# Kernel optimization log

Hardware: AMD Instinct MI355X
Metric: run time of the kernel (lower is better)

## Reference

```python
import jax, jax.numpy as jnp
import numpy as np

B, WS, DIM, HEADS, AGENT, PS = 128, 14, 256, 8, 49, 7
N = WS * WS


def conv(x, w, b, pad, groups=1):
    y = jax.lax.conv_general_dilated(x, w, (1, 1), [(pad, pad), (pad, pad)],
                                     dimension_numbers=('NCHW', 'OIHW', 'NCHW'),
                                     feature_group_count=groups)
    return y + b[None, :, None, None]


def bilinear_resize(x, oh, ow):
    # F.interpolate(mode='bilinear', align_corners=False) on last two dims
    ih, iw = x.shape[-2], x.shape[-1]
    def grid(ni, no):
        pos = np.maximum((np.arange(no) + 0.5) * (ni / no) - 0.5, 0.0)
        i0 = np.minimum(np.floor(pos).astype(np.int32), ni - 1)
        i1 = np.minimum(i0 + 1, ni - 1)
        return i0, i1, (pos - i0).astype(np.float32)
    i0h, i1h, lh = grid(ih, oh)
    i0w, i1w, lw = grid(iw, ow)
    xh = x[..., i0h, :] * (1.0 - lh)[:, None] + x[..., i1h, :] * lh[:, None]
    return xh[..., i0w] * (1.0 - lw) + xh[..., i1w] * lw


def rel_pos_index(h, w):
    coords = np.stack(np.meshgrid(np.arange(h), np.arange(w), indexing='ij')).reshape(2, -1)
    rel = (coords[:, :, None] - coords[:, None, :]).transpose(1, 2, 0).copy()
    rel[..., 0] += h - 1
    rel[..., 1] += w - 1
    rel[..., 0] *= 2 * w - 1
    return rel.sum(-1)  # (h*w, h*w)


def cbam(x, caa1_w, caa1_b, caa2_w, caa2_b, cam1_w, cam1_b, cam2_w, cam2_b, sa_w, sa_b):
    # ChannelAttention: both conv stacks act on 1x1 pooled maps -> only kernel centers matter
    avgp = x.mean((2, 3))
    t1 = jax.nn.relu(jnp.einsum('oi,bi->bo', caa1_w[:, :, 1, 1], avgp) + caa1_b)
    y1 = jax.nn.sigmoid(jnp.einsum('oi,bi->bo', caa2_w[:, :, 1, 1], t1) + caa2_b)
    mxp = x.max((2, 3))
    t2 = jax.nn.relu(jnp.einsum('oi,bi->bo', cam1_w[:, :, 0, 0], mxp) + cam1_b)
    y2 = jax.nn.sigmoid(jnp.einsum('oi,bi->bo', cam2_w[:, :, 0, 0], t2) + cam2_b)
    x = jax.nn.sigmoid(y1 + y2)[:, :, None, None] * x
    # Spatial attention
    mask = jnp.concatenate([x.mean(1, keepdims=True), x.max(1, keepdims=True)], axis=1)
    mask = jax.nn.sigmoid(conv(mask, sa_w, sa_b, 4))
    return x * mask


def chan_inter(x, ci1_w, ci1_b, bn_g, bn_b, ci2_w, ci2_b):
    # AdaptiveAvgPool2d(1) then 5x5 convs on 1x1 maps -> kernel-center matmuls; BN in eval mode
    p = x.mean((2, 3))
    t = jnp.einsum('oi,bi->bo', ci1_w[:, :, 2, 2], p) + ci1_b
    t = jax.nn.relu(bn_g * t * (1.0 / np.sqrt(1.0 + 1e-5)) + bn_b)
    return jnp.einsum('oi,bi->bo', ci2_w[:, :, 2, 2], t) + ci2_b


def setup_inputs() -> dict:
    key = jax.random.key(0)
    ks = jax.random.split(key, 40)
    d, r = DIM, DIM // 16
    p = lambda i, shape, s=0.02: jax.random.normal(ks[i], shape, jnp.float32) * s
    return {
        'x': jax.random.normal(ks[0], (B, N, d), jnp.float32),
        'h': WS,
        'w': WS,
        'lka_w': p(1, (3 * d, 1, 5, 5)), 'lka_b': p(2, (3 * d,)),
        'conv5_w': p(3, (d, d, 5, 5)), 'conv5_b': p(4, (d,)),
        'caa1_w': p(5, (r, d, 3, 3)), 'caa1_b': p(6, (r,)),
        'caa2_w': p(7, (d, r, 3, 3)), 'caa2_b': p(8, (d,)),
        'cam1_w': p(9, (r, d, 1, 1)), 'cam1_b': p(10, (r,)),
        'cam2_w': p(11, (d, r, 1, 1)), 'cam2_b': p(12, (d,)),
        'sa_w': p(13, (1, 2, 9, 9)), 'sa_b': p(14, (1,)),
        'ci1_w': p(15, (r, d, 5, 5)), 'ci1_b': p(16, (r,)),
        'bn_g': jnp.ones((r,), jnp.float32), 'bn_b': jnp.zeros((r,), jnp.float32),
        'ci2_w': p(17, (d, r, 5, 5)), 'ci2_b': p(18, (d,)),
        'rpb_table': p(19, ((2 * WS - 1) * (2 * WS - 1), HEADS)),
        'an_bias': p(20, (HEADS, AGENT, 7, 7)), 'na_bias': p(21, (HEADS, AGENT, 7, 7)),
        'ah_bias': p(22, (1, HEADS, AGENT, WS, 1)), 'aw_bias': p(23, (1, HEADS, AGENT, 1, WS)),
        'ha_bias': p(24, (1, HEADS, WS, 1, AGENT)), 'wa_bias': p(25, (1, HEADS, 1, WS, AGENT)),
        'dwc_w': p(26, (d, 1, 5, 5)), 'dwc_b': p(27, (d,)),
        'proj_w': p(28, (d, d)), 'proj_b': p(29, (d,)),
    }


def reference(x, h, w, lka_w, lka_b, conv5_w, conv5_b, caa1_w, caa1_b, caa2_w, caa2_b,
              cam1_w, cam1_b, cam2_w, cam2_b, sa_w, sa_b, ci1_w, ci1_b, bn_g, bn_b,
              ci2_w, ci2_b, rpb_table, an_bias, na_bias, ah_bias, aw_bias, ha_bias,
              wa_bias, dwc_w, dwc_b, proj_w, proj_b):
    b, n, c = x.shape
    heads, agent, ps = HEADS, AGENT, PS
    hd = c // heads
    scale = hd ** (-0.5)

    xc = jnp.transpose(x.reshape(b, h, w, c), (0, 3, 1, 2))  # (b,c,h,w)
    y = conv(xc, lka_w, lka_b, 2, groups=c)                   # depthwise, 3 outputs/group
    k_raw, v_raw, q_raw = y[:, :c], y[:, c:2 * c], y[:, 2 * c:]

    # v branch: conv5 then raw reshape-scramble (faithful to torch .reshape of NCHW), then CBAM
    v5 = jnp.transpose(conv(v_raw, conv5_w, conv5_b, 2).reshape(b, h, w, c), (0, 3, 1, 2))
    vc = cbam(v5, caa1_w, caa1_b, caa2_w, caa2_b, cam1_w, cam1_b, cam2_w, cam2_b, sa_w, sa_b)
    v_feat = jnp.transpose(vc.reshape(b, c, n), (0, 2, 1))    # (b,n,c)

    # adaptive avg/max pool 14->7 == exact 2x2 pooling
    at = q_raw.reshape(b, c, ps, h // ps, ps, w // ps).mean((3, 5)).reshape(b, c, agent).transpose(0, 2, 1)
    atk = k_raw.reshape(b, c, ps, h // ps, ps, w // ps).max((3, 5)).reshape(b, c, agent).transpose(0, 2, 1)

    # raw row-major reshapes of (b,c,h,w) into (b,n,heads,hd): faithful to torch
    q = q_raw.reshape(b, n, heads, hd).transpose(0, 2, 1, 3) * scale
    k = k_raw.reshape(b, n, heads, hd).transpose(0, 2, 1, 3)
    v = v_raw.reshape(b, n, heads, hd).transpose(0, 2, 1, 3)
    v1 = v_feat.reshape(b, n, heads, hd).transpose(0, 2, 1, 3)

    # full window attention with relative position bias
    idx = rel_pos_index(h, w)
    rpb = rpb_table[idx.reshape(-1)].reshape(n, n, heads).transpose(2, 0, 1)
    attn = jax.nn.softmax(jnp.einsum('bhid,bhjd->bhij', q, k) + rpb[None])
    x1 = jnp.einsum('bhij,bhjd->bhid', attn, v).transpose(0, 2, 1, 3).reshape(b, n, c)

    ar = x1.transpose(0, 2, 1).reshape(b, c, h, w)
    cmap = chan_inter(ar, ci1_w, ci1_b, bn_g, bn_b, ci2_w, ci2_b)  # (b,c)
    conv_x2 = jax.nn.sigmoid(cmap)[:, :, None, None] * jnp.transpose(q.reshape(b, h, w, c), (0, 3, 1, 2))

    # agent attention
    at_h = at.reshape(b, agent, heads, hd).transpose(0, 2, 1, 3)
    atk_h = atk.reshape(b, agent, heads, hd).transpose(0, 2, 1, 3)
    pb = bilinear_resize(an_bias, h, w).reshape(1, heads, agent, n) \
         + (ah_bias + aw_bias).reshape(1, heads, agent, n)
    agent_attn = jax.nn.softmax(jnp.einsum('bhad,bhnd->bhan', at_h * scale, k) + pb)
    agent_attn1 = jax.nn.softmax(jnp.einsum('bhad,bhnd->bhan', atk_h * scale, q) + pb)
    agent_v = jnp.einsum('bhan,bhnd->bhad', agent_attn, v1) + jnp.einsum('bhan,bhnd->bhad', agent_attn1, v)

    ab = bilinear_resize(na_bias, h, w).reshape(1, heads, agent, n).transpose(0, 1, 3, 2) \
         + (ha_bias + wa_bias).reshape(1, heads, n, agent)
    q_attn = jax.nn.softmax(jnp.einsum('bhnd,bhad->bhna', q * scale, at_h) + ab)
    k_attn = jax.nn.softmax(jnp.einsum('bhnd,bhad->bhna', k * scale, atk_h) + ab)
    xo = jnp.einsum('bhna,bhad->bhnd', q_attn + k_attn, agent_v).transpose(0, 2, 1, 3).reshape(b, n, c)

    xo = xo + jnp.transpose(conv(conv_x2, dwc_w, dwc_b, 2, groups=c), (0, 2, 3, 1)).reshape(b, n, c)
    qc = jnp.transpose(q.transpose(0, 2, 1, 3).reshape(b, h, w, c), (0, 3, 1, 2))
    xo = xo + jnp.transpose(conv(qc, dwc_w, dwc_b, 2, groups=c), (0, 2, 3, 1)).reshape(b, n, c)

    return xo @ proj_w.T + proj_b
```

## Files before the change

### kernel.cpp

```cpp
#include <hip/hip_runtime.h>

#define NB    128
#define NC    256
#define NPOS  196
#define NHEAD 8
#define NAG   49
#define YSTR  150528
#define VOFF  50176
#define QOFF  100352
#define SCL   0.17677669529663687f

#define WS_Y    0u
#define WS_V5   19267584u
#define WS_AT   25690112u
#define WS_ATK  27295744u
#define WS_CHG  28901376u
#define WS_CMAP 28934144u
#define WS_PBT  28966912u
#define WS_AB   29043744u
#define WS_X1S  29120576u
#define WS_AGV  29153344u
#define WS_XO   30758976u
#define WS_WT   37181504u
#define WS_CWT  37247040u

typedef __attribute__((ext_vector_type(8))) _Float16 half8;
typedef __attribute__((ext_vector_type(8))) short short8;
typedef __attribute__((ext_vector_type(4))) short short4v;
typedef __attribute__((ext_vector_type(4))) float f32x4;
typedef unsigned short ushort_t;
typedef unsigned int uint_t;

__device__ __forceinline__ float sigmoidf_(float x){ return 1.0f/(1.0f+__expf(-x)); }

__device__ __forceinline__ ushort_t f2h(float x){
  _Float16 h = (_Float16)x; return __builtin_bit_cast(ushort_t, h);
}
__device__ __forceinline__ float h2f(ushort_t u){
  return (float)__builtin_bit_cast(_Float16, u);
}

__device__ __forceinline__ float bilin7(const float* __restrict__ src, int i, int j){
  float pi = fmaxf(0.5f*(float)i - 0.25f, 0.f);
  int i0 = (int)pi; if (i0 > 6) i0 = 6;
  int i1 = i0 + 1;  if (i1 > 6) i1 = 6;
  float li = pi - (float)i0;
  float pj = fmaxf(0.5f*(float)j - 0.25f, 0.f);
  int j0 = (int)pj; if (j0 > 6) j0 = 6;
  int j1 = j0 + 1;  if (j1 > 6) j1 = 6;
  float lj = pj - (float)j0;
  float v00 = src[i0*7+j0], v01 = src[i0*7+j1];
  float v10 = src[i1*7+j0], v11 = src[i1*7+j1];
  float t0 = v00*(1.f-lj) + v01*lj;
  float t1 = v10*(1.f-lj) + v11*lj;
  return t0*(1.f-li) + t1*li;
}

__device__ __forceinline__ void conv5x5_row(const float* __restrict__ plane, int r,
                                            const float* __restrict__ w25, float* acc14){
  #pragma unroll
  for (int di = 0; di < 5; ++di){
    const float4* pr = (const float4*)(plane + (r+di)*20);
    float4 p0 = pr[0], p1 = pr[1], p2 = pr[2], p3 = pr[3], p4 = pr[4];
    float row[20] = {p0.x,p0.y,p0.z,p0.w, p1.x,p1.y,p1.z,p1.w, p2.x,p2.y,p2.z,p2.w,
                     p3.x,p3.y,p3.z,p3.w, p4.x,p4.y,p4.z,p4.w};
    #pragma unroll
    for (int dj = 0; dj < 5; ++dj){
      float w = w25[di*5+dj];
      #pragma unroll
      for (int j = 0; j < 14; ++j) acc14[j] = fmaf(row[j+dj], w, acc14[j]);
    }
  }
}

__global__ void k_pbab(const float* __restrict__ an, const float* __restrict__ ah,
                       const float* __restrict__ aw, const float* __restrict__ na,
                       const float* __restrict__ ha, const float* __restrict__ wa,
                       float* __restrict__ PBT, float* __restrict__ AB){
  int bid = blockIdx.x;
  int which = (bid >= 301);
  int t = (which ? bid - 301 : bid)*256 + threadIdx.x;
  if (t >= NHEAD*NPOS*NAG) return;
  int a = t % NAG;
  int r = t / NAG;
  int n = r % NPOS;
  int h = r / NPOS;
  int i = n/14, j = n - (n/14)*14;
  if (!which){
    float v = bilin7(an + ((size_t)h*NAG + a)*49, i, j);
    v += ah[((size_t)h*NAG + a)*14 + i] + aw[((size_t)h*NAG + a)*14 + j];
    PBT[t] = v;
  } else {
    float v = bilin7(na + ((size_t)h*NAG + a)*49, i, j);
    v += ha[((size_t)h*14 + i)*NAG + a] + wa[((size_t)h*14 + j)*NAG + a];
    AB[t] = v;
  }
}

__global__ void k_wt(const float* __restrict__ pw, float* __restrict__ WT){
  int t = blockIdx.x*256 + threadIdx.x;
  if (t >= 65536) return;
  int k = t >> 8, c = t & 255;
  WT[t] = pw[c*256 + k];
}

__global__ void k_cw2(const float* __restrict__ cw, ushort_t* __restrict__ Wh){
  int t = blockIdx.x*256 + threadIdx.x;
  if (t >= 1638400) return;
  int ci = t & 255;
  int r  = t >> 8;
  int co = r & 255;
  int tap = r >> 8;
  Wh[t] = f2h(cw[((size_t)co*256 + ci)*25 + tap]);
}

__global__ __launch_bounds__(256) void k_lka(const float* __restrict__ x, const float* __restrict__ lw,
                                             const float* __restrict__ lb, float* __restrict__ Y){
  int b = blockIdx.x >> 3, gb = blockIdx.x & 7;
  int g0 = gb*32;
  __shared__ __align__(16) float pl[32*360];
  int tid = threadIdx.x;
  for (int t = tid; t < 32*360; t += 256) pl[t] = 0.f;
  __syncthreads();
  for (int t = tid; t < 32*196; t += 256){
    int gl = t & 31, s = t >> 5;
    int i = s/14, j = s - i*14;
    pl[gl*360 + (i+2)*20 + j + 2] = x[((size_t)b*196 + s)*256 + g0 + gl];
  }
  __syncthreads();
  for (int t = tid; t < 96*14; t += 256){
    int ocl = t/14, r = t - ocl*14;
    int o  = g0*3 + ocl;
    int gl = ocl/3;
    float w25[25];
    #pragma unroll
    for (int u = 0; u < 25; ++u) w25[u] = lw[o*25 + u];
    float acc[14];
    float bv = lb[o];
    #pragma unroll
    for (int j = 0; j < 14; ++j) acc[j] = bv;
    conv5x5_row(&pl[gl*360], r, w25, acc);
    float* dst = Y + ((size_t)b*768 + o)*196 + r*14;
    #pragma unroll
    for (int j = 0; j < 14; ++j) dst[j] = acc[j];
  }
}

__global__ __launch_bounds__(256, 2) void k_conv5(const float* __restrict__ Y,
    const ushort_t* __restrict__ Wh, const float* __restrict__ cb, float* __restrict__ V5){
  int b = blockIdx.x >> 2, cog = blockIdx.x & 3;
  int co0 = cog*64;
  __shared__ __align__(16) ushort_t Pt[360*40];
  __shared__ __align__(16) ushort_t Wsm[2*5*64*40];
  float* T = (float*)Wsm;
  int tid  = threadIdx.x;
  int lane = tid & 63, wv = tid >> 6;
  int mrow = lane & 15, quad = lane >> 4;

  for (int t = tid; t < 7200; t += 256) ((uint_t*)Pt)[t] = 0;

  int prow[4];
  #pragma unroll
  for (int mt = 0; mt < 4; ++mt){
    int s = wv*64 + mt*16 + mrow;
    int p0 = 0;
    if (s < 196){ int i = s/14, j = s - i*14; p0 = i*20 + j; }
    prow[mt] = p0;
  }

  f32x4 acc[4][4];
  #pragma unroll
  for (int mt = 0; mt < 4; ++mt)
    #pragma unroll
    for (int nt = 0; nt < 4; ++nt) acc[mt][nt] = (f32x4){0.f,0.f,0.f,0.f};

  const float* src = Y + (size_t)b*YSTR + VOFF;
  int wco = tid >> 2, wpart = tid & 3;
  const ushort_t* wbase = Wh + ((size_t)(co0 + wco))*256 + wpart*8;

  short8 wreg[5];
  #pragma unroll
  for (int tp = 0; tp < 5; ++tp)
    wreg[tp] = *(const short8*)(wbase + (size_t)tp*65536);

  #pragma unroll 1
  for (int cc = 0; cc < 8; ++cc){
    __syncthreads();
    for (int t = tid; t < 784; t += 256){
      int pos = t >> 2, ch = t & 3;
      int i = pos/14, j = pos - i*14;
      int p = (i+2)*20 + j + 2;
      const float* s0 = src + (size_t)(cc*32 + ch*8)*196 + pos;
      short8 pk;
      #pragma unroll
      for (int e = 0; e < 4; ++e){
        float v0 = s0[(2*e)*196];
        float v1 = s0[(2*e+1)*196];
        pk[2*e]   = (short)f2h(v0);
        pk[2*e+1] = (short)f2h(v1);
      }
      *(short8*)&Pt[p*40 + ch*8] = pk;
    }
    #pragma unroll 1
    for (int di = 0; di < 5; ++di){
      int u = cc*5 + di;
      ushort_t* wbuf = Wsm + (u & 1)*12800;
      #pragma unroll
      for (int tp = 0; tp < 5; ++tp)
        *(short8*)&wbuf[(tp*64 + wco)*40 + wpart*8] = wreg[tp];
      if (u < 39){
        int di1 = di + 1, cc1 = cc;
        if (di1 == 5){ di1 = 0; ++cc1; }
        #pragma unroll
        for (int tp = 0; tp < 5; ++tp)
          wreg[tp] = *(const short8*)(wbase + (size_t)(di1*5 + tp)*65536 + cc1*32);
      }
      __syncthreads();
      #pragma unroll
      for (int dj = 0; dj < 5; ++dj){
        half8 a[4], bb[4];
        #pragma unroll
        for (int nt = 0; nt < 4; ++nt){
          int co = nt*16 + mrow;
          bb[nt] = *(const half8*)&wbuf[(dj*64 + co)*40 + quad*8];
        }
        #pragma unroll
        for (int mt = 0; mt < 4; ++mt){
          int p = prow[mt] + di*20 + dj;
          a[mt] = *(const half8*)&Pt[p*40 + quad*8];
        }
        #pragma unroll
        for (int mt = 0; mt < 4; ++mt)
          #pragma unroll
          for (int nt = 0; nt < 4; ++nt)
            acc[mt][nt] = __builtin_amdgcn_mfma_f32_16x16x32_f16(a[mt], bb[nt], acc[mt][nt], 0, 0, 0);
      }
    }
  }

  #pragma unroll
  for (int hf = 0; hf < 2; ++hf){
    __syncthreads();
    #pragma unroll
    for (int ntl = 0; ntl < 2; ++ntl){
      int nt = hf*2 + ntl;
      int col = ntl*16 + mrow;
      #pragma unroll
      for (int mt = 0; mt < 4; ++mt){
        int sbase = wv*64 + mt*16 + quad*4;
        #pragma unroll
        for (int r = 0; r < 4; ++r){
          int s = sbase + r;
          if (s < 196) T[col*200 + s] = acc[mt][nt][r];
        }
      }
    }
    __syncthreads();
    for (int t = tid; t < 6272; t += 256){
      int cl = t / 196;
      int f = (co0 + hf*32)*196 + t;
      float val = T[t + cl*4] + cb[co0 + hf*32 + cl];
      V5[(size_t)b*50176 + (size_t)(f & 255)*196 + (f >> 8)] = val;
    }
  }
}

__global__ __launch_bounds__(256) void k_pool(const float* __restrict__ Y, float* __restrict__ AT, float* __restrict__ ATK){
  int b = blockIdx.x >> 1, half = blockIdx.x & 1;
  int c = (threadIdx.x & 127) + half*128;
  int a0 = (threadIdx.x >> 7) ? 25 : 0;
  int a1 = (threadIdx.x >> 7) ? 49 : 25;
  const float* qp = Y + ((size_t)b*768 + 512 + c)*196;
  const float* kp = Y + ((size_t)b*768 + c)*196;
  for (int a = a0; a < a1; ++a){
    int p1 = a/7, p2 = a - p1*7;
    int s = p1*28 + p2*2;
    float q0 = qp[s], q1 = qp[s+1], q2 = qp[s+14], q3 = qp[s+15];
    AT[((size_t)b*49 + a)*256 + c] = 0.25f*(q0+q1+q2+q3);
    float k0 = kp[s], k1 = kp[s+1], k2 = kp[s+14], k3 = kp[s+15];
    ATK[((size_t)b*49 + a)*256 + c] = fmaxf(fmaxf(k0,k1), fmaxf(k2,k3));
  }
}

__global__ __launch_bounds__(256) void k_cbam_a(const float* __restrict__ V5,
    const float* __restrict__ caa1w, const float* __restrict__ caa1b,
    const float* __restrict__ caa2w, const float* __restrict__ caa2b,
    const float* __restrict__ cam1w, const float* __restrict__ cam1b,
    const float* __restrict__ cam2w, const float* __restrict__ cam2b,
    float* __restrict__ CHG){
  int b = blockIdx.x, c = threadIdx.x;
  __shared__ float avg[256], mx[256], t1[16], t2[16];
  const float* pp = V5 + ((size_t)b*256 + c)*196;
  float s = 0.f, m = -1e30f;
  for (int i = 0; i < 196; ++i){ float v = pp[i]; s += v; m = fmaxf(m, v); }
  avg[c] = s * (1.0f/196.0f); mx[c] = m;
  __syncthreads();
  if (c < 16){
    float a1 = caa1b[c], a2 = cam1b[c];
    #pragma unroll 4
    for (int k = 0; k < 256; ++k){
      a1 = fmaf(caa1w[(c*256 + k)*9 + 4], avg[k], a1);
      a2 = fmaf(cam1w[c*256 + k], mx[k], a2);
    }
    t1[c] = fmaxf(a1, 0.f);
    t2[c] = fmaxf(a2, 0.f);
  }
  __syncthreads();
  float y1 = caa2b[c], y2 = cam2b[c];
  #pragma unroll
  for (int k = 0; k < 16; ++k){
    y1 = fmaf(caa2w[(c*16 + k)*9 + 4], t1[k], y1);
    y2 = fmaf(cam2w[c*16 + k], t2[k], y2);
  }
  CHG[b*256 + c] = sigmoidf_(sigmoidf_(y1) + sigmoidf_(y2));
}

__global__ __launch_bounds__(256) void k_cbam_b(float* __restrict__ V5, const float* __restrict__ CHG,
    const float* __restrict__ saw, const float* __restrict__ sab){
  int b = blockIdx.x; int tid = threadIdx.x;
  __shared__ float chg[256];
  __shared__ float mp[22*22], xp[22*22];
  __shared__ float mk[196];
  chg[tid] = CHG[b*256 + tid];
  for (int t = tid; t < 484; t += 256){ mp[t] = 0.f; xp[t] = 0.f; }
  __syncthreads();
  if (tid < 196){
    int i = tid/14, j = tid - i*14;
    float s = 0.f, m = -1e30f;
    const float* vb = V5 + (size_t)b*256*196 + tid;
    for (int c = 0; c < 256; ++c){
      float v = chg[c] * vb[c*196];
      s += v; m = fmaxf(m, v);
    }
    mp[(i+4)*22 + j+4] = s*(1.f/256.f);
    xp[(i+4)*22 + j+4] = m;
  }
  __syncthreads();
  if (tid < 196){
    int i = tid/14, j = tid - i*14;
    float acc = sab[0];
    for (int di = 0; di < 9; ++di){
      #pragma unroll
      for (int dj = 0; dj < 9; ++dj){
        acc = fmaf(mp[(i+di)*22 + j+dj], saw[di*9+dj], acc);
        acc = fmaf(xp[(i+di)*22 + j+dj], saw[81 + di*9+dj], acc);
      }
    }
    mk[tid] = sigmoidf_(acc);
  }
  __syncthreads();
  if (tid < 196){
    float m = mk[tid];
    float* vb = V5 + (size_t)b*256*196 + tid;
    for (int c = 0; c < 256; ++c) vb[c*196] = chg[c]*vb[c*196]*m;
  }
}

__global__ __launch_bounds__(512, 4) void k_attn3(const float* __restrict__ Y,
    const float* __restrict__ rpbt, float* __restrict__ X1S){
  int b = blockIdx.x >> 3, h = blockIdx.x & 7;
  __shared__ __align__(16) ushort_t Qh[208*32];
  __shared__ __align__(16) ushort_t Kh[208*32];
  __shared__ __align__(16) ushort_t E[80*208];
  __shared__ float rp[736];
  __shared__ int   rpo[208];
  __shared__ float pl2[80][2];
  __shared__ float invl[80];
  __shared__ float wj[208];
  __shared__ float wpart[8][208];
  __shared__ float xpart[16][32];
  int tid = threadIdx.x, wv = tid >> 6, lane = tid & 63;
  int mrow = lane & 15, quad = lane >> 4;
  int sw8 = ((quad ^ ((mrow >> 1) & 3)) << 3);
  const float* yb = Y + (size_t)b*YSTR;

  for (int t = tid; t < 736; t += 512) rp[t] = (t < 729) ? rpbt[t*8 + h] : 0.f;
  for (int j = tid; j < 208; j += 512){
    int jc = (j < 196) ? j : 195;
    int rj = jc/14;
    rpo[j] = rj*27 + (jc - rj*14);
    wj[j] = 0.f;
  }
  for (int t = tid; t < 384; t += 512){
    int arr = t >= 192; int u = t - arr*192;
    ((uint_t*)(arr ? Kh : Qh))[3136 + u] = 0;
  }
  for (int t = tid; t < 3136; t += 512){
    int n = t >> 4, w = t & 15;
    int ws = (((w >> 2) ^ ((n >> 1) & 3)) << 2) | (w & 3);
    const float2 qv = *(const float2*)(yb + QOFF + (size_t)n*256 + h*32 + (w << 1));
    ((uint_t*)Qh)[n*16 + ws] = (uint_t)f2h(qv.x*SCL) | ((uint_t)f2h(qv.y*SCL) << 16);
    const float2 kv = *(const float2*)(yb + (size_t)n*256 + h*32 + (w << 1));
    ((uint_t*)Kh)[n*16 + ws] = (uint_t)f2h(kv.x) | ((uint_t)f2h(kv.y) << 16);
  }
  __syncthreads();

  int mt0 = (wv & 1) ? 7 : 0;
  int mt1 = (wv & 1) ? 13 : 7;

  #pragma unroll 1
  for (int seg = 0; seg < 3; ++seg){
    int base = (seg == 0) ? 0 : (seg == 1) ? 80 : 144;
    int ntl  = (seg == 0) ? 5 : 4;
    int segrows = ntl*16;
    int vrows = 196 - base; if (vrows > segrows) vrows = segrows;

    #pragma unroll 1
    for (int ncl = (wv >> 1); ncl < ntl; ncl += 4){
      int n = base + ncl*16 + mrow;
      half8 bfr = *(const half8*)&Qh[n*32 + sw8];
      int nclamp = (n < 196) ? n : 195;
      int rin = nclamp/14, cin = nclamp - rin*14;
      int bidxn = (rin + 13)*27 + (cin + 13);
      float lsum = 0.f;
      #pragma unroll 1
      for (int mt = mt0; mt < mt1; ++mt){
        half8 afr = *(const half8*)&Kh[(mt*16 + mrow)*32 + sw8];
        f32x4 c = (f32x4){0.f,0.f,0.f,0.f};
        c = __builtin_amdgcn_mfma_f32_16x16x32_f16(afr, bfr, c, 0, 0, 0);
        int j0 = mt*16 + quad*4;
        int4 ro = *(const int4*)&rpo[j0];
        short4v pk;
        #pragma unroll
        for (int r = 0; r < 4; ++r){
          int j = j0 + r;
          int roff = (r == 0) ? ro.x : (r == 1) ? ro.y : (r == 2) ? ro.z : ro.w;
          float e = (j < 196) ? __expf(c[r] + rp[bidxn - roff]) : 0.f;
          lsum += e;
          pk[r] = (short)f2h(e);
        }
        if (n < 196) *(short4v*)&E[(n - base)*208 + j0] = pk;
      }
      lsum += __shfl_xor(lsum, 16);
      lsum += __shfl_xor(lsum, 32);
      if (quad == 0) pl2[n - base][wv & 1] = lsum;
    }
    __syncthreads();
    for (int t = tid; t < vrows; t += 512) invl[t] = 1.f/(pl2[t][0] + pl2[t][1]);
    __syncthreads();

    {
      int j0 = lane*4;
      if (j0 < 208){
        float a0=0.f,a1=0.f,a2=0.f,a3=0.f;
        #pragma unroll 1
        for (int nl = wv; nl < vrows; nl += 8){
          float iv = invl[nl];
          short4v ev = *(const short4v*)&E[nl*208 + j0];
          a0 = fmaf(h2f((ushort_t)ev[0]), iv, a0);
          a1 = fmaf(h2f((ushort_t)ev[1]), iv, a1);
          a2 = fmaf(h2f((ushort_t)ev[2]), iv, a2);
          a3 = fmaf(h2f((ushort_t)ev[3]), iv, a3);
        }
        *(f32x4*)&wpart[wv][j0] = (f32x4){a0,a1,a2,a3};
      }
    }
    __syncthreads();
    for (int j = tid; j < 208; j += 512){
      float s = wj[j];
      #pragma unroll
      for (int g = 0; g < 8; ++g) s += wpart[g][j];
      wj[j] = s;
    }
    __syncthreads();
  }

  {
    int d = tid & 31, g = tid >> 5;
    float s = 0.f;
    #pragma unroll 1
    for (int u = 0; u < 13; ++u){
      int j = g*13 + u;
      s = fmaf(wj[j], yb[VOFF + (size_t)j*256 + h*32 + d], s);
    }
    xpart[g][d] = s;
  }
  __syncthreads();
  if (tid < 32){
    float s = 0.f;
    #pragma unroll
    for (int g2 = 0; g2 < 16; ++g2) s += xpart[g2][tid];
    X1S[(size_t)b*256 + h*32 + tid] = s*(1.f/196.f);
  }
}

__global__ __launch_bounds__(256) void k_cinter(const float* __restrict__ X1S,
    const float* __restrict__ ci1w, const float* __restrict__ ci1b,
    const float* __restrict__ bng, const float* __restrict__ bnb,
    const float* __restrict__ ci2w, const float* __restrict__ ci2b, float* __restrict__ CMAP){
  int b = blockIdx.x, c = threadIdx.x;
  __shared__ float p[256], tt[16];
  p[c] = X1S[b*256 + c];
  __syncthreads();
  if (c < 16){
    float a = ci1b[c];
    #pragma unroll 4
    for (int k = 0; k < 256; ++k) a = fmaf(ci1w[(c*256+k)*25 + 12], p[k], a);
    const float invs = 0.9999950000375f;
    tt[c] = fmaxf(fmaf(bng[c]*invs, a, bnb[c]), 0.f);
  }
  __syncthreads();
  float a = ci2b[c];
  #pragma unroll
  for (int k = 0; k < 16; ++k) a = fmaf(ci2w[(c*16+k)*25 + 12], tt[k], a);
  CMAP[b*256 + c] = sigmoidf_(a);
}

__global__ __launch_bounds__(256) void k_agentv(const float* __restrict__ Y, const float* __restrict__ V5,
    const float* __restrict__ AT, const float* __restrict__ ATK,
    const float* __restrict__ PBT, float* __restrict__ AGV){
  int b = blockIdx.x >> 3, h = blockIdx.x & 7;
  __shared__ __align__(16) ushort_t ST[64*232];
  __shared__ __align__(16) ushort_t R[8704];
  __shared__ float psum[4*64];
  __shared__ float inv0s[64], inv1s[64];
  int tid = threadIdx.x, wv = tid >> 6, lane = tid & 63;
  int mrow = lane & 15, quad = lane >> 4;
  int sw8 = ((quad ^ ((mrow >> 1) & 3)) << 3);
  const float* yb = Y + (size_t)b*YSTR;
  ushort_t* Kh = R;
  ushort_t* Ah = R + 6656;
  ushort_t* Vt = R;
  f32x4 out0[2], out1[2];

  for (int t = tid; t < 512; t += 256){
    int a = t >> 3, c2 = 208 + ((t & 7) << 1);
    *(uint_t*)&ST[a*232 + c2] = 0;
  }

  #pragma unroll 1
  for (int pass = 0; pass < 2; ++pass){
    for (int t = tid; t < 192; t += 256) ((uint_t*)Kh)[3136 + t] = 0;
    for (int t = tid; t < 240; t += 256) ((uint_t*)Ah)[784 + t] = 0;
    {
      const float* rsrc = yb + (pass ? QOFF : 0) + h*32;
      for (int t = tid; t < 3136; t += 256){
        int n = t >> 4, w = t & 15;
        const float2 v = *(const float2*)(rsrc + (size_t)n*256 + (w << 1));
        int ws = (((w >> 2) ^ ((n >> 1) & 3)) << 2) | (w & 3);
        ((uint_t*)Kh)[n*16 + ws] = (uint_t)f2h(v.x) | ((uint_t)f2h(v.y) << 16);
      }
      const float* asrc = (pass ? ATK : AT) + (size_t)b*49*256 + h*32;
      for (int t = tid; t < 784; t += 256){
        int a = t >> 4, w = t & 15;
        const float2 v = *(const float2*)(asrc + (size_t)a*256 + (w << 1));
        int ws = (((w >> 2) ^ ((a >> 1) & 3)) << 2) | (w & 3);
        ((uint_t*)Ah)[a*16 + ws] = (uint_t)f2h(v.x) | ((uint_t)f2h(v.y) << 16);
      }
    }
    __syncthreads();
    {
      float lscl = pass ? 0.03125f : SCL;
      int ag = wv*16 + mrow;
      half8 bfr = *(const half8*)&Ah[ag*32 + sw8];
      #pragma unroll 1
      for (int mt = 0; mt < 13; ++mt){
        half8 afr = *(const half8*)&Kh[(mt*16 + mrow)*32 + sw8];
        f32x4 c = (f32x4){0.f,0.f,0.f,0.f};
        c = __builtin_amdgcn_mfma_f32_16x16x32_f16(afr, bfr, c, 0, 0, 0);
        int n0 = mt*16 + quad*4;
        short4v pk;
        #pragma unroll
        for (int r = 0; r < 4; ++r){
          int n = n0 + r;
          float pb = PBT[((size_t)h*196 + n)*49 + ag];
          float e = (n < 196) ? __expf(fmaf(c[r], lscl, pb)) : 0.f;
          pk[r] = (short)f2h(e);
        }
        *(short4v*)&ST[ag*232 + n0] = pk;
      }
    }
    __syncthreads();
    {
      int a = tid >> 2, q = tid & 3;
      float s = 0.f;
      #pragma unroll
      for (int u = 0; u < 7; ++u){
        short8 v8 = *(const short8*)&ST[a*232 + q*56 + u*8];
        #pragma unroll
        for (int e = 0; e < 8; ++e) s += h2f((ushort_t)v8[e]);
      }
      psum[q*64 + a] = s;
    }
    if (pass == 0){
      const float* vsrc = V5 + (size_t)b*50176 + h*32*196;
      for (int t = tid; t < 3136; t += 256){
        int d = t / 98, np = t - (t/98)*98;
        const float2 v = *(const float2*)(vsrc + (size_t)d*196 + 2*np);
        *(uint_t*)&Vt[d*232 + 2*np] = (uint_t)f2h(v.x) | ((uint_t)f2h(v.y) << 16);
      }
    } else {
      const float* vsrc = yb + VOFF + h*32;
      for (int t = tid; t < 3136; t += 256){
        int d = t / 98, np = t - (t/98)*98;
        float v0 = vsrc[(size_t)(2*np)*256 + d];
        float v1 = vsrc[(size_t)(2*np+1)*256 + d];
        *(uint_t*)&Vt[d*232 + 2*np] = (uint_t)f2h(v0) | ((uint_t)f2h(v1) << 16);
      }
    }
    for (int t = tid; t < 448; t += 256){
      int d = t / 14, c2 = 196 + 2*(t - (t/14)*14);
      *(uint_t*)&Vt[d*232 + c2] = 0;
    }
    __syncthreads();
    {
      f32x4* outp = pass ? out1 : out0;
      #pragma unroll
      for (int nt = 0; nt < 2; ++nt){
        f32x4 c = (f32x4){0.f,0.f,0.f,0.f};
        #pragma unroll
        for (int ks = 0; ks < 7; ++ks){
          half8 afr = *(const half8*)&ST[(wv*16 + mrow)*232 + ks*32 + quad*8];
          half8 bfr = *(const half8*)&Vt[(nt*16 + mrow)*232 + ks*32 + quad*8];
          c = __builtin_amdgcn_mfma_f32_16x16x32_f16(afr, bfr, c, 0, 0, 0);
        }
        outp[nt] = c;
      }
      if (tid < 64){
        float s = psum[tid] + psum[64+tid] + psum[128+tid] + psum[192+tid];
        float* invp = pass ? inv1s : inv0s;
        invp[tid] = 1.f / s;
      }
    }
    __syncthreads();
  }
  #pragma unroll
  for (int nt = 0; nt < 2; ++nt){
    int d = nt*16 + mrow;
    #pragma unroll
    for (int r = 0; r < 4; ++r){
      int a = wv*16 + quad*4 + r;
      if (a < 49)
        AGV[(((size_t)(b*8 + h)*49) + a)*32 + d] = out0[nt][r]*inv0s[a] + out1[nt][r]*inv1s[a];
    }
  }
}

__global__ __launch_bounds__(256) void k_xo1(const float* __restrict__ Y,
    const float* __restrict__ AT, const float* __restrict__ ATK,
    const float* __restrict__ AB, const float* __restrict__ AGV, float* __restrict__ XO){
  int b = blockIdx.x >> 3, h = blockIdx.x & 7;
  __shared__ __align__(16) ushort_t ST[208*72];
  __shared__ __align__(16) ushort_t Kh[208*32];
  __shared__ __align__(16) ushort_t Ah[64*32];
  __shared__ __align__(16) ushort_t AGVt[32*64];
  __shared__ float invs[208];
  int tid = threadIdx.x, wv = tid >> 6, lane = tid & 63;
  int mrow = lane & 15, quad = lane >> 4;
  int sw8 = ((quad ^ ((mrow >> 1) & 3)) << 3);
  const float* yb = Y + (size_t)b*YSTR;
  f32x4 acc[4][2];
  #pragma unroll
  for (int i = 0; i < 4; ++i){
    acc[i][0] = (f32x4){0.f,0.f,0.f,0.f};
    acc[i][1] = (f32x4){0.f,0.f,0.f,0.f};
  }

  for (int t = tid; t < 1664; t += 256){
    int rw = t >> 3, c2 = 48 + ((t & 7) << 1);
    *(uint_t*)&ST[rw*72 + c2] = 0;
  }
  {
    const float* agvb = AGV + (size_t)(b*8 + h)*49*32;
    for (int t = tid; t < 2048; t += 256){
      int d = t >> 6, a = t & 63;
      int as = ((((a >> 3) ^ (d & 7)) & 7) << 3) | (a & 7);
      AGVt[d*64 + as] = (a < 49) ? f2h(agvb[a*32 + d]) : (ushort_t)0;
    }
  }

  #pragma unroll 1
  for (int pass = 0; pass < 2; ++pass){
    {
      const float* rsrc = yb + (pass ? 0 : QOFF) + h*32;
      for (int t = tid; t < 3136; t += 256){
        int n = t >> 4, w = t & 15;
        const float2 v = *(const float2*)(rsrc + (size_t)n*256 + (w << 1));
        int ws = (((w >> 2) ^ ((n >> 1) & 3)) << 2) | (w & 3);
        ((uint_t*)Kh)[n*16 + ws] = (uint_t)f2h(v.x) | ((uint_t)f2h(v.y) << 16);
      }
      const float* asrc = (pass ? ATK : AT) + (size_t)b*49*256 + h*32;
      for (int t = tid; t < 784; t += 256){
        int a = t >> 4, w = t & 15;
        const float2 v = *(const float2*)(asrc + (size_t)a*256 + (w << 1));
        int ws = (((w >> 2) ^ ((a >> 1) & 3)) << 2) | (w & 3);
        ((uint_t*)Ah)[a*16 + ws] = (uint_t)f2h(v.x) | ((uint_t)f2h(v.y) << 16);
      }
    }
    __syncthreads();
    {
      float lscl = pass ? SCL : 0.03125f;
      int ag = wv*16 + mrow;
      half8 bfr = *(const half8*)&Ah[ag*32 + sw8];
      #pragma unroll 1
      for (int mt = 0; mt < 13; ++mt){
        half8 afr = *(const half8*)&Kh[(mt*16 + mrow)*32 + sw8];
        f32x4 c = (f32x4){0.f,0.f,0.f,0.f};
        c = __builtin_amdgcn_mfma_f32_16x16x32_f16(afr, bfr, c, 0, 0, 0);
        #pragma unroll
        for (int r = 0; r < 4; ++r){
          int n = mt*16 + quad*4 + r;
          if (n < 196 && ag < 49){
            float e = __expf(fmaf(c[r], lscl, AB[((size_t)h*196 + n)*49 + ag]));
            ST[n*72 + ag] = f2h(e);
          }
        }
      }
    }
    __syncthreads();
    if (tid < 196){
      float s = 0.f;
      #pragma unroll
      for (int u = 0; u < 7; ++u){
        short8 v8 = *(const short8*)&ST[tid*72 + u*8];
        #pragma unroll
        for (int e = 0; e < 8; ++e) s += h2f((ushort_t)v8[e]);
      }
      invs[tid] = 1.f / s;
    }
    __syncthreads();
    {
      int i = 0;
      #pragma unroll 1
      for (int mt = wv; mt < 13; mt += 4, ++i){
        #pragma unroll
        for (int nt = 0; nt < 2; ++nt){
          f32x4 c = (f32x4){0.f,0.f,0.f,0.f};
          #pragma unroll
          for (int ks = 0; ks < 2; ++ks){
            half8 afr = *(const half8*)&ST[(mt*16 + mrow)*72 + ks*32 + quad*8];
            half8 bfr = *(const half8*)&AGVt[(nt*16 + mrow)*64 + ((((ks*4 + quad) ^ (mrow & 7)) & 7) << 3)];
            c = __builtin_amdgcn_mfma_f32_16x16x32_f16(afr, bfr, c, 0, 0, 0);
          }
          #pragma unroll
          for (int r = 0; r < 4; ++r){
            int n = mt*16 + quad*4 + r;
            if (n < 196) acc[i][nt][r] = fmaf(c[r], invs[n], acc[i][nt][r]);
          }
        }
      }
    }
    __syncthreads();
  }
  {
    int i = 0;
    #pragma unroll 1
    for (int mt = wv; mt < 13; mt += 4, ++i){
      #pragma unroll
      for (int nt = 0; nt < 2; ++nt){
        #pragma unroll
        for (int r = 0; r < 4; ++r){
          int n = mt*16 + quad*4 + r;
          if (n < 196)
            XO[((size_t)b*196 + n)*256 + h*32 + nt*16 + mrow] = acc[i][nt][r];
        }
      }
    }
  }
}

__global__ __launch_bounds__(256) void k_dwc(const float* __restrict__ Y, const float* __restrict__ CMAP,
    const float* __restrict__ dw, const float* __restrict__ db, float* __restrict__ XO){
  int b = blockIdx.x >> 3, cg = blockIdx.x & 7;
  int c0 = cg*32;
  __shared__ __align__(16) float pl[32*360];
  int tid = threadIdx.x;
  for (int t = tid; t < 32*360; t += 256) pl[t] = 0.f;
  __syncthreads();
  const float* yq = Y + (size_t)b*YSTR + QOFF;
  for (int t = tid; t < 32*196; t += 256){
    int cl = t & 31, s = t >> 5;
    int c = c0 + cl;
    int G = s*256 + c;
    int hh = G / 6272;
    int rem = G - hh*6272;
    int n = rem >> 5, d = rem & 31;
    float cx2 = CMAP[b*256 + c] * yq[n*256 + hh*32 + d];
    float qc  = yq[G];
    float v = SCL*(cx2 + qc);
    int i = s/14, j = s - i*14;
    pl[cl*360 + (i+2)*20 + j + 2] = v;
  }
  __syncthreads();
  for (int t = tid; t < 32*14; t += 256){
    int cl = t/14, r = t - cl*14;
    int c = c0 + cl;
    float w25[25];
    #pragma unroll
    for (int u = 0; u < 25; ++u) w25[u] = dw[c*25 + u];
    float acc[14];
    float b2 = 2.f*db[c];
    #pragma unroll
    for (int j = 0; j < 14; ++j) acc[j] = b2;
    conv5x5_row(&pl[cl*360], r, w25, acc);
    float* dst = XO + ((size_t)b*196 + r*14)*256 + c;
    #pragma unroll
    for (int j = 0; j < 14; ++j) dst[j*256] += acc[j];
  }
}

__global__ __launch_bounds__(256) void k_proj(const float* __restrict__ XO, const float* __restrict__ WT,
    const float* __restrict__ pbias, float* __restrict__ OUT){
  int bb = blockIdx.x / 7, nt = blockIdx.x % 7;
  int n0 = nt*28;
  int c = threadIdx.x;
  const float* xb = XO + ((size_t)bb*196 + n0)*256;
  float acc[28];
  #pragma unroll
  for (int r = 0; r < 28; ++r) acc[r] = 0.f;
  for (int k = 0; k < 256; k += 4){
    float w0 = WT[(k+0)*256 + c];
    float w1 = WT[(k+1)*256 + c];
    float w2 = WT[(k+2)*256 + c];
    float w3 = WT[(k+3)*256 + c];
    #pragma unroll
    for (int r = 0; r < 28; ++r){
      float4 xv = *(const float4*)(xb + r*256 + k);
      acc[r] = fmaf(xv.x, w0, fmaf(xv.y, w1, fmaf(xv.z, w2, fmaf(xv.w, w3, acc[r]))));
    }
  }
  float bv = pbias[c];
  float* dst = OUT + ((size_t)bb*196 + n0)*256 + c;
  #pragma unroll
  for (int r = 0; r < 28; ++r) dst[r*256] = acc[r] + bv;
}

extern "C" void kernel_launch(void* const* d_in, const int* in_sizes, int n_in,
                              void* d_out, int out_size, void* d_ws, size_t ws_size,
                              hipStream_t stream){
  (void)in_sizes; (void)n_in; (void)out_size; (void)ws_size;
  const float* x       = (const float*)d_in[0];
  const float* lka_w   = (const float*)d_in[3];
  const float* lka_b   = (const float*)d_in[4];
  const float* conv5_w = (const float*)d_in[5];
  const float* conv5_b = (const float*)d_in[6];
  const float* caa1_w  = (const float*)d_in[7];
  const float* caa1_b  = (const float*)d_in[8];
  const float* caa2_w  = (const float*)d_in[9];
  const float* caa2_b  = (const float*)d_in[10];
  const float* cam1_w  = (const float*)d_in[11];
  const float* cam1_b  = (const float*)d_in[12];
  const float* cam2_w  = (const float*)d_in[13];
  const float* cam2_b  = (const float*)d_in[14];
  const float* sa_w    = (const float*)d_in[15];
  const float* sa_b    = (const float*)d_in[16];
  const float* ci1_w   = (const float*)d_in[17];
  const float* ci1_b   = (const float*)d_in[18];
  const float* bn_g    = (const float*)d_in[19];
  const float* bn_b    = (const float*)d_in[20];
  const float* ci2_w   = (const float*)d_in[21];
  const float* ci2_b   = (const float*)d_in[22];
  const float* rpbt    = (const float*)d_in[23];
  const float* an_bias = (const float*)d_in[24];
  const float* na_bias = (const float*)d_in[25];
  const float* ah_bias = (const float*)d_in[26];
  const float* aw_bias = (const float*)d_in[27];
  const float* ha_bias = (const float*)d_in[28];
  const float* wa_bias = (const float*)d_in[29];
  const float* dwc_w   = (const float*)d_in[30];
  const float* dwc_b   = (const float*)d_in[31];
  const float* proj_w  = (const float*)d_in[32];
  const float* proj_b  = (const float*)d_in[33];
  float* out = (float*)d_out;
  float* ws = (float*)d_ws;

  float* Y    = ws + WS_Y;
  float* V5   = ws + WS_V5;
  float* AT   = ws + WS_AT;
  float* ATK  = ws + WS_ATK;
  float* CHG  = ws + WS_CHG;
  float* CMAP = ws + WS_CMAP;
  float* PBT  = ws + WS_PBT;
  float* AB   = ws + WS_AB;
  float* X1S  = ws + WS_X1S;
  float* AGV  = ws + WS_AGV;
  float* XO   = ws + WS_XO;
  float* WT   = ws + WS_WT;
  ushort_t* Wh = (ushort_t*)(ws + WS_CWT);

  k_pbab <<<602, 256, 0, stream>>>(an_bias, ah_bias, aw_bias, na_bias, ha_bias, wa_bias, PBT, AB);
  k_wt   <<<256, 256, 0, stream>>>(proj_w, WT);
  k_cw2  <<<6400, 256, 0, stream>>>(conv5_w, Wh);
  k_lka  <<<1024, 256, 0, stream>>>(x, lka_w, lka_b, Y);
  k_conv5<<<512, 256, 0, stream>>>(Y, Wh, conv5_b, V5);
  k_pool <<<256, 256, 0, stream>>>(Y, AT, ATK);
  k_cbam_a<<<128, 256, 0, stream>>>(V5, caa1_w, caa1_b, caa2_w, caa2_b,
                                    cam1_w, cam1_b, cam2_w, cam2_b, CHG);
  k_cbam_b<<<128, 256, 0, stream>>>(V5, CHG, sa_w, sa_b);
  k_attn3<<<1024, 512, 0, stream>>>(Y, rpbt, X1S);
  k_cinter<<<128, 256, 0, stream>>>(X1S, ci1_w, ci1_b, bn_g, bn_b, ci2_w, ci2_b, CMAP);
  k_agentv<<<1024, 256, 0, stream>>>(Y, V5, AT, ATK, PBT, AGV);
  k_xo1  <<<1024, 256, 0, stream>>>(Y, AT, ATK, AB, AGV, XO);
  k_dwc  <<<1024, 256, 0, stream>>>(Y, CMAP, dwc_w, dwc_b, XO);
  k_proj <<<896, 256, 0, stream>>>(XO, WT, proj_b, out);
}
```

Baseline: 803.8 us.

## Merge weight-prep and CBAM kernels, vectorize reductions and V transpose loads

```diff
diff --git a/kernel.cpp b/kernel.cpp
--- a/kernel.cpp
+++ b/kernel.cpp
@@ -97,21 +97,25 @@
   }
 }
 
-__global__ void k_wt(const float* __restrict__ pw, float* __restrict__ WT){
-  int t = blockIdx.x*256 + threadIdx.x;
-  if (t >= 65536) return;
-  int k = t >> 8, c = t & 255;
-  WT[t] = pw[c*256 + k];
-}
-
-__global__ void k_cw2(const float* __restrict__ cw, ushort_t* __restrict__ Wh){
-  int t = blockIdx.x*256 + threadIdx.x;
-  if (t >= 1638400) return;
-  int ci = t & 255;
-  int r  = t >> 8;
-  int co = r & 255;
-  int tap = r >> 8;
-  Wh[t] = f2h(cw[((size_t)co*256 + ci)*25 + tap]);
+__global__ void k_wprep(const float* __restrict__ cw, ushort_t* __restrict__ Wh,
+                        const float* __restrict__ pw, float* __restrict__ WT){
+  int bid = blockIdx.x;
+  if (bid < 800){
+    int base = (bid*256 + threadIdx.x)*8;
+    int r   = base >> 8;
+    int co  = r & 255;
+    int tap = r >> 8;
+    int ci0 = base & 255;
+    const float* srcb = cw + (size_t)co*6400 + (size_t)ci0*25 + tap;
+    short8 o;
+    #pragma unroll
+    for (int e = 0; e < 8; ++e) o[e] = (short)f2h(srcb[e*25]);
+    *(short8*)(Wh + base) = o;
+  } else {
+    int t = (bid - 800)*256 + threadIdx.x;
+    int k = t >> 8, c = t & 255;
+    WT[t] = pw[c*256 + k];
+  }
 }
 
 __global__ __launch_bounds__(256) void k_lka(const float* __restrict__ x, const float* __restrict__ lw,
@@ -282,52 +286,63 @@
   }
 }
 
-__global__ __launch_bounds__(256) void k_cbam_a(const float* __restrict__ V5,
+__global__ __launch_bounds__(256) void k_cbam(float* __restrict__ V5,
     const float* __restrict__ caa1w, const float* __restrict__ caa1b,
     const float* __restrict__ caa2w, const float* __restrict__ caa2b,
     const float* __restrict__ cam1w, const float* __restrict__ cam1b,
     const float* __restrict__ cam2w, const float* __restrict__ cam2b,
-    float* __restrict__ CHG){
-  int b = blockIdx.x, c = threadIdx.x;
-  __shared__ float avg[256], mx[256], t1[16], t2[16];
-  const float* pp = V5 + ((size_t)b*256 + c)*196;
-  float s = 0.f, m = -1e30f;
-  for (int i = 0; i < 196; ++i){ float v = pp[i]; s += v; m = fmaxf(m, v); }
-  avg[c] = s * (1.0f/196.0f); mx[c] = m;
-  __syncthreads();
-  if (c < 16){
-    float a1 = caa1b[c], a2 = cam1b[c];
+    const float* __restrict__ saw, const float* __restrict__ sab){
+  int b = blockIdx.x;
+  __shared__ float avg[256], mx[256], t1[16], t2[16], chg[256];
+  __shared__ float mp[22*22], xp[22*22];
+  __shared__ float mk[196];
+  int tid = threadIdx.x, wv = tid >> 6, lane = tid & 63;
+  float* v5b = V5 + (size_t)b*50176;
+
+  for (int t = tid; t < 484; t += 256){ mp[t] = 0.f; xp[t] = 0.f; }
+
+  for (int c = wv; c < 256; c += 4){
+    float s, m;
+    if (lane < 49){
+      float4 v = *(const float4*)(v5b + c*196 + lane*4);
+      s = v.x + v.y + v.z + v.w;
+      m = fmaxf(fmaxf(v.x, v.y), fmaxf(v.z, v.w));
+    } else { s = 0.f; m = -1e30f; }
+    #pragma unroll
+    for (int off = 1; off < 64; off <<= 1){
+      s += __shfl_xor(s, off);
+      m = fmaxf(m, __shfl_xor(m, off));
+    }
+    if (lane == 0){ avg[c] = s*(1.0f/196.0f); mx[c] = m; }
+  }
+  __syncthreads();
+
+  if (tid < 16){
+    float a1 = caa1b[tid], a2 = cam1b[tid];
     #pragma unroll 4
     for (int k = 0; k < 256; ++k){
-      a1 = fmaf(caa1w[(c*256 + k)*9 + 4], avg[k], a1);
-      a2 = fmaf(cam1w[c*256 + k], mx[k], a2);
-    }
-    t1[c] = fmaxf(a1, 0.f);
-    t2[c] = fmaxf(a2, 0.f);
-  }
-  __syncthreads();
-  float y1 = caa2b[c], y2 = cam2b[c];
-  #pragma unroll
-  for (int k = 0; k < 16; ++k){
-    y1 = fmaf(caa2w[(c*16 + k)*9 + 4], t1[k], y1);
-    y2 = fmaf(cam2w[c*16 + k], t2[k], y2);
-  }
-  CHG[b*256 + c] = sigmoidf_(sigmoidf_(y1) + sigmoidf_(y2));
-}
-
-__global__ __launch_bounds__(256) void k_cbam_b(float* __restrict__ V5, const float* __restrict__ CHG,
-    const float* __restrict__ saw, const float* __restrict__ sab){
-  int b = blockIdx.x; int tid = threadIdx.x;
-  __shared__ float chg[256];
-  __shared__ float mp[22*22], xp[22*22];
-  __shared__ float mk[196];
-  chg[tid] = CHG[b*256 + tid];
-  for (int t = tid; t < 484; t += 256){ mp[t] = 0.f; xp[t] = 0.f; }
-  __syncthreads();
+      a1 = fmaf(caa1w[(tid*256 + k)*9 + 4], avg[k], a1);
+      a2 = fmaf(cam1w[tid*256 + k], mx[k], a2);
+    }
+    t1[tid] = fmaxf(a1, 0.f);
+    t2[tid] = fmaxf(a2, 0.f);
+  }
+  __syncthreads();
+  {
+    float y1 = caa2b[tid], y2 = cam2b[tid];
+    #pragma unroll
+    for (int k = 0; k < 16; ++k){
+      y1 = fmaf(caa2w[(tid*16 + k)*9 + 4], t1[k], y1);
+      y2 = fmaf(cam2w[tid*16 + k], t2[k], y2);
+    }
+    chg[tid] = sigmoidf_(sigmoidf_(y1) + sigmoidf_(y2));
+  }
+  __syncthreads();
+
   if (tid < 196){
     int i = tid/14, j = tid - i*14;
     float s = 0.f, m = -1e30f;
-    const float* vb = V5 + (size_t)b*256*196 + tid;
+    const float* vb = v5b + tid;
     for (int c = 0; c < 256; ++c){
       float v = chg[c] * vb[c*196];
       s += v; m = fmaxf(m, v);
@@ -351,7 +366,7 @@
   __syncthreads();
   if (tid < 196){
     float m = mk[tid];
-    float* vb = V5 + (size_t)b*256*196 + tid;
+    float* vb = v5b + tid;
     for (int c = 0; c < 256; ++c) vb[c*196] = chg[c]*vb[c*196]*m;
   }
 }
@@ -592,10 +607,10 @@
     } else {
       const float* vsrc = yb + VOFF + h*32;
       for (int t = tid; t < 3136; t += 256){
-        int d = t / 98, np = t - (t/98)*98;
-        float v0 = vsrc[(size_t)(2*np)*256 + d];
-        float v1 = vsrc[(size_t)(2*np+1)*256 + d];
-        *(uint_t*)&Vt[d*232 + 2*np] = (uint_t)f2h(v0) | ((uint_t)f2h(v1) << 16);
+        int np = t >> 4, dp = t & 15;
+        const float2 v = *(const float2*)(vsrc + (size_t)np*256 + (dp << 1));
+        Vt[(2*dp)*232 + np]     = f2h(v.x);
+        Vt[(2*dp + 1)*232 + np] = f2h(v.y);
       }
     }
     for (int t = tid; t < 448; t += 256){
@@ -868,7 +883,6 @@
   float* V5   = ws + WS_V5;
   float* AT   = ws + WS_AT;
   float* ATK  = ws + WS_ATK;
-  float* CHG  = ws + WS_CHG;
   float* CMAP = ws + WS_CMAP;
   float* PBT  = ws + WS_PBT;
   float* AB   = ws + WS_AB;
@@ -879,14 +893,12 @@
   ushort_t* Wh = (ushort_t*)(ws + WS_CWT);
 
   k_pbab <<<602, 256, 0, stream>>>(an_bias, ah_bias, aw_bias, na_bias, ha_bias, wa_bias, PBT, AB);
-  k_wt   <<<256, 256, 0, stream>>>(proj_w, WT);
-  k_cw2  <<<6400, 256, 0, stream>>>(conv5_w, Wh);
+  k_wprep<<<1056, 256, 0, stream>>>(conv5_w, Wh, proj_w, WT);
   k_lka  <<<1024, 256, 0, stream>>>(x, lka_w, lka_b, Y);
   k_conv5<<<512, 256, 0, stream>>>(Y, Wh, conv5_b, V5);
   k_pool <<<256, 256, 0, stream>>>(Y, AT, ATK);
-  k_cbam_a<<<128, 256, 0, stream>>>(V5, caa1_w, caa1_b, caa2_w, caa2_b,
-                                    cam1_w, cam1_b, cam2_w, cam2_b, CHG);
-  k_cbam_b<<<128, 256, 0, stream>>>(V5, CHG, sa_w, sa_b);
+  k_cbam <<<128, 256, 0, stream>>>(V5, caa1_w, caa1_b, caa2_w, caa2_b,
+                                   cam1_w, cam1_b, cam2_w, cam2_b, sa_w, sa_b);
   k_attn3<<<1024, 512, 0, stream>>>(Y, rpbt, X1S);
   k_cinter<<<128, 256, 0, stream>>>(X1S, ci1_w, ci1_b, bn_g, bn_b, ci2_w, ci2_b, CMAP);
   k_agentv<<<1024, 256, 0, stream>>>(Y, V5, AT, ATK, PBT, AGV);
```

After: 794.9 us. About the same (-1.1%).
